# Performance work log

Hardware: AMD Instinct MI355X
Metric: run time of the kernel (lower is better)

## Reference

```python
import jax, jax.numpy as jnp
import numpy as np

QUALITY = 50.0
TEMP = 0.3  # soft-round temperature

_LUM = np.array([[16,11,10,16,24,40,51,61],[12,12,14,19,26,58,60,55],[14,13,16,24,40,57,69,56],[14,17,22,29,51,87,80,62],[18,22,37,56,68,109,103,77],[24,35,55,64,81,104,113,92],[49,64,78,87,103,121,120,101],[72,92,95,98,112,100,103,99]], dtype=np.float32)
_CHR = np.array([[17,18,24,47,99,99,99,99],[18,21,26,66,99,99,99,99],[24,26,56,99,99,99,99,99],[47,66,99,99,99,99,99,99],[99,99,99,99,99,99,99,99],[99,99,99,99,99,99,99,99],[99,99,99,99,99,99,99,99],[99,99,99,99,99,99,99,99]], dtype=np.float32)

def _scaled_qtable(base, qf):
    qf = max(1.0, min(100.0, qf))
    s = 5000.0 / qf if qf < 50 else 200.0 - 2.0 * qf
    return np.maximum(np.floor((base * s + 50.0) / 100.0), 1.0)

# Per-channel quantization tables: Y uses luminance, Cb/Cr use chrominance. (3,8,8)
QTAB = jnp.asarray(np.stack([_scaled_qtable(_LUM, QUALITY), _scaled_qtable(_CHR, QUALITY), _scaled_qtable(_CHR, QUALITY)]).astype(np.float32))

# The original 64x1x8x8 conv kernel factors as outer product D[u,x]*D[v,y].
_u = np.arange(8)[:, None]
_x = np.arange(8)[None, :]
_c = np.where(_u == 0, 1.0 / np.sqrt(2.0), 1.0)
DCT = jnp.asarray((0.5 * _c * np.cos((2 * _x + 1) * _u * np.pi / 16.0)).astype(np.float32))

M_FWD = jnp.array([[0.299, 0.587, 0.114], [-0.168736, -0.331264, 0.5], [0.5, -0.418688, -0.081312]], dtype=jnp.float32)
M_INV = jnp.array([[1.0, 0.0, 1.402], [1.0, -0.344136, -0.714136], [1.0, 1.772, 0.0]], dtype=jnp.float32)
OFF = jnp.array([0.0, 0.5, 0.5], dtype=jnp.float32)


def setup_inputs() -> dict:
    key = jax.random.key(0)
    x = jax.random.uniform(key, (32, 3, 512, 512), dtype=jnp.float32)
    return {"x": x}


def reference(x):
    B, C, H, W = x.shape  # H, W divisible by 8 (no pad branch)
    # RGB -> YCbCr, centered
    ycbcr = jnp.einsum('ij,bjhw->bihw', M_FWD, x) + OFF[None, :, None, None] - 0.5
    # split into 8x8 blocks: (B, 3, H/8, 8, W/8, 8)
    blocks = ycbcr.reshape(B, C, H // 8, 8, W // 8, 8)
    # block DCT: coef[u,v] = sum_{x,y} D[u,x] D[v,y] block[x,y]
    coef = jnp.einsum('ux,vy,bchxgy->bchugv', DCT, DCT, blocks)
    q = QTAB[None, :, None, :, None, :]  # broadcast per-channel table
    d = coef / q
    # smooth rounding: x + 0.5*tanh(50*T*(x - round(x)))
    sr = d + 0.5 * jnp.tanh(50.0 * TEMP * (d - jnp.round(d)))
    deq = sr * q
    # block IDCT (transpose of DCT): block[x,y] = sum_{u,v} D[u,x] D[v,y] coef[u,v]
    rec = jnp.einsum('ux,vy,bchugv->bchxgy', DCT, DCT, deq)
    ycbcr_rec = rec.reshape(B, C, H, W) + 0.5
    rgb = jnp.einsum('ij,bjhw->bihw', M_INV, ycbcr_rec - OFF[None, :, None, None])
    return jnp.clip(rgb, 0.0, 1.0)
```

## Files before the change

kernel.cpp:

```cpp
#include <hip/hip_runtime.h>
#include <math.h>

#define A0c 0.35355339059327373f
#define C1c 0.4903926402016152f
#define C2c 0.46193976625564337f
#define C3c 0.41573480615127262f
#define C5c 0.27778511650980114f
#define C6c 0.19134171618254492f
#define C7c 0.09754516100806417f

#define IMG_W 512
#define IMG_HW (512 * 512)

typedef float f8v __attribute__((ext_vector_type(8)));

__device__ const float QLUMT[64] = {
    16,12,14,14,18,24,49,72,
    11,12,13,17,22,35,64,92,
    10,14,16,22,37,55,78,95,
    16,19,24,29,56,64,87,98,
    24,26,40,51,68,81,103,112,
    40,58,57,87,109,104,121,100,
    51,60,69,80,103,113,120,103,
    61,55,56,62,77,92,101,99};
__device__ const float QCHRT[64] = {
    17,18,24,47,99,99,99,99,
    18,21,26,66,99,99,99,99,
    24,26,56,99,99,99,99,99,
    47,66,99,99,99,99,99,99,
    99,99,99,99,99,99,99,99,
    99,99,99,99,99,99,99,99,
    99,99,99,99,99,99,99,99,
    99,99,99,99,99,99,99,99};

__device__ __forceinline__ void fdct8(float v[8]) {
    float s0 = v[0] + v[7], s1 = v[1] + v[6], s2 = v[2] + v[5], s3 = v[3] + v[4];
    float d0 = v[0] - v[7], d1 = v[1] - v[6], d2 = v[2] - v[5], d3 = v[3] - v[4];
    float e0 = s0 + s3, e1 = s1 + s2, f0 = s0 - s3, f1 = s1 - s2;
    v[0] = A0c * (e0 + e1);
    v[4] = A0c * (e0 - e1);
    v[2] = C2c * f0 + C6c * f1;
    v[6] = C6c * f0 - C2c * f1;
    v[1] = C1c * d0 + C3c * d1 + C5c * d2 + C7c * d3;
    v[3] = C3c * d0 - C7c * d1 - C1c * d2 - C5c * d3;
    v[5] = C5c * d0 - C1c * d1 + C7c * d2 + C3c * d3;
    v[7] = C7c * d0 - C5c * d1 + C3c * d2 - C1c * d3;
}

__device__ __forceinline__ void idct8(float v[8]) {
    float g0 = v[0], g1 = v[1], g2 = v[2], g3 = v[3];
    float g4 = v[4], g5 = v[5], g6 = v[6], g7 = v[7];
    float ep = A0c * (g0 + g4), em = A0c * (g0 - g4);
    float t26a = C2c * g2 + C6c * g6;
    float t26b = C6c * g2 - C2c * g6;
    float e0 = ep + t26a, e1 = em + t26b, e2 = em - t26b, e3 = ep - t26a;
    float o0 = C1c * g1 + C3c * g3 + C5c * g5 + C7c * g7;
    float o1 = C3c * g1 - C7c * g3 - C1c * g5 - C5c * g7;
    float o2 = C5c * g1 - C1c * g3 + C7c * g5 + C3c * g7;
    float o3 = C7c * g1 - C5c * g3 + C3c * g5 - C1c * g7;
    v[0] = e0 + o0; v[7] = e0 - o0;
    v[1] = e1 + o1; v[6] = e1 - o1;
    v[2] = e2 + o2; v[5] = e2 - o2;
    v[3] = e3 + o3; v[4] = e3 - o3;
}

__device__ __forceinline__ float softq(float x, float q, float rq) {
    float d = x * rq;
    float rn = rintf(d);
    float t = d - rn;
    float e = __expf(-30.0f * fabsf(t));
    float th = (1.0f - e) * __builtin_amdgcn_rcpf(1.0f + e);
    th = copysignf(th, t);
    return (d + 0.5f * th) * q;
}

__device__ __forceinline__ void midchain(float w[8], const f8v q, const f8v rq) {
    fdct8(w);
#pragma unroll
    for (int u = 0; u < 8; ++u) w[u] = softq(w[u], q[u], rq[u]);
    idct8(w);
}

__device__ __forceinline__ void process_tile(const f8v Rv, const f8v Gv, const f8v Bv,
                                             float* xp0, float* xp1, float* xp2,
                                             int wi, int ri,
                                             const f8v qL, const f8v rqL,
                                             const f8v qC, const f8v rqC,
                                             float* obase) {
    float g0[8], g1[8], g2[8];
#pragma unroll
    for (int k = 0; k < 8; ++k) {
        float R = Rv[k], G = Gv[k], B = Bv[k];
        g0[k] = 0.299f * R + 0.587f * G + 0.114f * B - 0.5f;
        g1[k] = -0.168736f * R - 0.331264f * G + 0.5f * B;
        g2[k] = 0.5f * R - 0.418688f * G - 0.081312f * B;
    }
    fdct8(g0); fdct8(g1); fdct8(g2);

#pragma unroll
    for (int v = 0; v < 8; ++v) xp0[v * 72 + wi] = g0[v];
#pragma unroll
    for (int v = 0; v < 8; ++v) xp1[v * 72 + wi] = g1[v];
#pragma unroll
    for (int v = 0; v < 8; ++v) xp2[v * 72 + wi] = g2[v];

#pragma unroll
    for (int k = 0; k < 8; ++k) g0[k] = xp0[ri + k];
#pragma unroll
    for (int k = 0; k < 8; ++k) g1[k] = xp1[ri + k];
#pragma unroll
    for (int k = 0; k < 8; ++k) g2[k] = xp2[ri + k];

    midchain(g0, qL, rqL);
#pragma unroll
    for (int k = 0; k < 8; ++k) xp0[ri + k] = g0[k];
    midchain(g1, qC, rqC);
#pragma unroll
    for (int k = 0; k < 8; ++k) xp1[ri + k] = g1[k];
#pragma unroll
    for (int v = 0; v < 8; ++v) g0[v] = xp0[v * 72 + wi];
    midchain(g2, qC, rqC);
#pragma unroll
    for (int k = 0; k < 8; ++k) xp2[ri + k] = g2[k];
#pragma unroll
    for (int v = 0; v < 8; ++v) g1[v] = xp1[v * 72 + wi];
#pragma unroll
    for (int v = 0; v < 8; ++v) g2[v] = xp2[v * 72 + wi];

    idct8(g0); idct8(g1); idct8(g2);

    f8v Ro, Go, Bo;
#pragma unroll
    for (int k = 0; k < 8; ++k) {
        float Y  = g0[k] + 0.5f;
        float Cb = g1[k];
        float Cr = g2[k];
        float R = Y + 1.402f * Cr;
        float G = Y - 0.344136f * Cb - 0.714136f * Cr;
        float B = Y + 1.772f * Cb;
        Ro[k] = fminf(fmaxf(R, 0.0f), 1.0f);
        Go[k] = fminf(fmaxf(G, 0.0f), 1.0f);
        Bo[k] = fminf(fmaxf(B, 0.0f), 1.0f);
    }
    *(f8v*)(obase) = Ro;
    *(f8v*)(obase + IMG_HW) = Go;
    *(f8v*)(obase + 2 * IMG_HW) = Bo;
}

__global__ __launch_bounds__(256) void jpeg_kernel(const float* __restrict__ x,
                                                   float* __restrict__ out) {
    __shared__ float xpose[4][3][576];

    const int tid = threadIdx.x;
    const int wid = tid >> 6;
    const int lane = tid & 63;

    const int gw = blockIdx.x * 4 + wid;
    const int bimg = gw >> 9;
    const int rem = gw & 511;
    const int gh = rem >> 3;
    const int tx = rem & 7;

    const int blk = lane & 7;
    const int row = lane >> 3;

    const size_t off = (size_t)bimg * 3 * IMG_HW +
                       (size_t)(gh * 8 + row) * IMG_W + tx * 64 + blk * 8;
    const size_t toff = (size_t)16 * 3 * IMG_HW;

    const float* base0 = x + off;
    const float* base1 = base0 + toff;

    const f8v R0 = *(const f8v*)(base0);
    const f8v G0 = *(const f8v*)(base0 + IMG_HW);
    const f8v B0 = *(const f8v*)(base0 + 2 * IMG_HW);
    const f8v R1 = *(const f8v*)(base1);
    const f8v G1 = *(const f8v*)(base1 + IMG_HW);
    const f8v B1 = *(const f8v*)(base1 + 2 * IMG_HW);
    const f8v qL = *(const f8v*)&QLUMT[row * 8];
    const f8v qC = *(const f8v*)&QCHRT[row * 8];

    asm volatile("" ::: "memory");

    f8v rqL, rqC;
#pragma unroll
    for (int u = 0; u < 8; ++u) {
        rqL[u] = __builtin_amdgcn_rcpf(qL[u]);
        rqC[u] = __builtin_amdgcn_rcpf(qC[u]);
    }

    float* xp0 = xpose[wid][0];
    float* xp1 = xpose[wid][1];
    float* xp2 = xpose[wid][2];
    const int wi = blk * 9 + row;
    const int ri = row * 72 + blk * 9;

    process_tile(R0, G0, B0, xp0, xp1, xp2, wi, ri, qL, rqL, qC, rqC, out + off);
    process_tile(R1, G1, B1, xp0, xp1, xp2, wi, ri, qL, rqL, qC, rqC, out + off + toff);
}

extern "C" void kernel_launch(void* const* d_in, const int* in_sizes, int n_in,
                              void* d_out, int out_size, void* d_ws, size_t ws_size,
                              hipStream_t stream) {
    const float* x = (const float*)d_in[0];
    float* out = (float*)d_out;
    const int n_wg = 2048;
    hipLaunchKernelGGL(jpeg_kernel, dim3(n_wg), dim3(256), 0, stream, x, out);
}
```

Baseline: 39.89 us.

## Transpose 8x8 blocks in registers via DPP/swizzle instead of shared memory

Replaces the shared-memory transpose between row and column DCT passes with an in-register 8x8 transpose built from DPP row shuffles and ds_swizzle across the 8 lanes that hold a block. Lane mapping changes so each group of 8 consecutive lanes owns one block, and each thread now handles one tile instead of two, doubling the grid size. The soft-round tanh is also simplified to a single exp2-based expression without abs/copysign. The goal is to drop LDS traffic and its latency, at the cost of extra cross-lane moves and selects, and less per-thread load batching.

```diff
diff --git a/kernel.cpp b/kernel.cpp
--- a/kernel.cpp
+++ b/kernel.cpp
@@ -64,29 +64,74 @@
     v[3] = e3 + o3; v[4] = e3 - o3;
 }
 
+#define K_EXP2 43.2808512266689f
 __device__ __forceinline__ float softq(float x, float q, float rq) {
     float d = x * rq;
     float rn = rintf(d);
     float t = d - rn;
-    float e = __expf(-30.0f * fabsf(t));
-    float th = (1.0f - e) * __builtin_amdgcn_rcpf(1.0f + e);
-    th = copysignf(th, t);
+    float e2 = __builtin_amdgcn_exp2f(K_EXP2 * t);
+    float th = (e2 - 1.0f) * __builtin_amdgcn_rcpf(e2 + 1.0f);
     return (d + 0.5f * th) * q;
 }
 
-__device__ __forceinline__ void midchain(float w[8], const f8v q, const f8v rq) {
-    fdct8(w);
-#pragma unroll
-    for (int u = 0; u < 8; ++u) w[u] = softq(w[u], q[u], rq[u]);
-    idct8(w);
+template <int CTRL>
+__device__ __forceinline__ float fdpp(float x) {
+    return __int_as_float(__builtin_amdgcn_mov_dpp(__float_as_int(x), CTRL, 0xF, 0xF, false));
+}
+__device__ __forceinline__ float fswz4(float x) {
+    return __int_as_float(__builtin_amdgcn_ds_swizzle(__float_as_int(x), 0x101F));
 }
 
-__device__ __forceinline__ void process_tile(const f8v Rv, const f8v Gv, const f8v Bv,
-                                             float* xp0, float* xp1, float* xp2,
-                                             int wi, int ri,
-                                             const f8v qL, const f8v rqL,
-                                             const f8v qC, const f8v rqC,
-                                             float* obase) {
+__device__ __forceinline__ void xpose8(float v[8], bool rb0, bool rb1, bool rb2) {
+    float t[8];
+#pragma unroll
+    for (int i = 0; i < 8; ++i) t[i] = fdpp<0xB1>(v[i ^ 1]);
+#pragma unroll
+    for (int i = 0; i < 8; ++i) v[i] = (((i & 1) != 0) == rb0) ? v[i] : t[i];
+#pragma unroll
+    for (int i = 0; i < 8; ++i) t[i] = fdpp<0x4E>(v[i ^ 2]);
+#pragma unroll
+    for (int i = 0; i < 8; ++i) v[i] = (((i & 2) != 0) == rb1) ? v[i] : t[i];
+#pragma unroll
+    for (int i = 0; i < 8; ++i) t[i] = fswz4(v[i ^ 4]);
+#pragma unroll
+    for (int i = 0; i < 8; ++i) v[i] = (((i & 4) != 0) == rb2) ? v[i] : t[i];
+}
+
+__global__ __launch_bounds__(256) void jpeg_kernel(const float* __restrict__ x,
+                                                   float* __restrict__ out) {
+    const int tid = threadIdx.x;
+    const int wid = tid >> 6;
+    const int lane = tid & 63;
+
+    const int gw = blockIdx.x * 4 + wid;
+    const int bimg = gw >> 9;
+    const int rem = gw & 511;
+    const int gh = rem >> 3;
+    const int tx = rem & 7;
+
+    const int r = lane & 7;
+    const int blk = lane >> 3;
+
+    const bool rb0 = (r & 1) != 0, rb1 = (r & 2) != 0, rb2 = (r & 4) != 0;
+
+    const size_t off = (size_t)bimg * 3 * IMG_HW +
+                       (size_t)(gh * 8 + r) * IMG_W + tx * 64 + blk * 8;
+    const float* base = x + off;
+
+    const f8v Rv = *(const f8v*)(base);
+    const f8v Gv = *(const f8v*)(base + IMG_HW);
+    const f8v Bv = *(const f8v*)(base + 2 * IMG_HW);
+
+    const f8v qL = *(const f8v*)&QLUMT[r * 8];
+    const f8v qC = *(const f8v*)&QCHRT[r * 8];
+    f8v rqL, rqC;
+#pragma unroll
+    for (int u = 0; u < 8; ++u) {
+        rqL[u] = __builtin_amdgcn_rcpf(qL[u]);
+        rqC[u] = __builtin_amdgcn_rcpf(qC[u]);
+    }
+
     float g0[8], g1[8], g2[8];
 #pragma unroll
     for (int k = 0; k < 8; ++k) {
@@ -95,39 +140,33 @@
         g1[k] = -0.168736f * R - 0.331264f * G + 0.5f * B;
         g2[k] = 0.5f * R - 0.418688f * G - 0.081312f * B;
     }
-    fdct8(g0); fdct8(g1); fdct8(g2);
 
+    fdct8(g0);
+    xpose8(g0, rb0, rb1, rb2);
+    fdct8(g0);
 #pragma unroll
-    for (int v = 0; v < 8; ++v) xp0[v * 72 + wi] = g0[v];
+    for (int u = 0; u < 8; ++u) g0[u] = softq(g0[u], qL[u], rqL[u]);
+    idct8(g0);
+    xpose8(g0, rb0, rb1, rb2);
+    idct8(g0);
+
+    fdct8(g1);
+    xpose8(g1, rb0, rb1, rb2);
+    fdct8(g1);
 #pragma unroll
-    for (int v = 0; v < 8; ++v) xp1[v * 72 + wi] = g1[v];
+    for (int u = 0; u < 8; ++u) g1[u] = softq(g1[u], qC[u], rqC[u]);
+    idct8(g1);
+    xpose8(g1, rb0, rb1, rb2);
+    idct8(g1);
+
+    fdct8(g2);
+    xpose8(g2, rb0, rb1, rb2);
+    fdct8(g2);
 #pragma unroll
-    for (int v = 0; v < 8; ++v) xp2[v * 72 + wi] = g2[v];
-
-#pragma unroll
-    for (int k = 0; k < 8; ++k) g0[k] = xp0[ri + k];
-#pragma unroll
-    for (int k = 0; k < 8; ++k) g1[k] = xp1[ri + k];
-#pragma unroll
-    for (int k = 0; k < 8; ++k) g2[k] = xp2[ri + k];
-
-    midchain(g0, qL, rqL);
-#pragma unroll
-    for (int k = 0; k < 8; ++k) xp0[ri + k] = g0[k];
-    midchain(g1, qC, rqC);
-#pragma unroll
-    for (int k = 0; k < 8; ++k) xp1[ri + k] = g1[k];
-#pragma unroll
-    for (int v = 0; v < 8; ++v) g0[v] = xp0[v * 72 + wi];
-    midchain(g2, qC, rqC);
-#pragma unroll
-    for (int k = 0; k < 8; ++k) xp2[ri + k] = g2[k];
-#pragma unroll
-    for (int v = 0; v < 8; ++v) g1[v] = xp1[v * 72 + wi];
-#pragma unroll
-    for (int v = 0; v < 8; ++v) g2[v] = xp2[v * 72 + wi];
-
-    idct8(g0); idct8(g1); idct8(g2);
+    for (int u = 0; u < 8; ++u) g2[u] = softq(g2[u], qC[u], rqC[u]);
+    idct8(g2);
+    xpose8(g2, rb0, rb1, rb2);
+    idct8(g2);
 
     f8v Ro, Go, Bo;
 #pragma unroll
@@ -142,61 +181,10 @@
         Go[k] = fminf(fmaxf(G, 0.0f), 1.0f);
         Bo[k] = fminf(fmaxf(B, 0.0f), 1.0f);
     }
+    float* obase = out + off;
     *(f8v*)(obase) = Ro;
     *(f8v*)(obase + IMG_HW) = Go;
     *(f8v*)(obase + 2 * IMG_HW) = Bo;
-}
-
-__global__ __launch_bounds__(256) void jpeg_kernel(const float* __restrict__ x,
-                                                   float* __restrict__ out) {
-    __shared__ float xpose[4][3][576];
-
-    const int tid = threadIdx.x;
-    const int wid = tid >> 6;
-    const int lane = tid & 63;
-
-    const int gw = blockIdx.x * 4 + wid;
-    const int bimg = gw >> 9;
-    const int rem = gw & 511;
-    const int gh = rem >> 3;
-    const int tx = rem & 7;
-
-    const int blk = lane & 7;
-    const int row = lane >> 3;
-
-    const size_t off = (size_t)bimg * 3 * IMG_HW +
-                       (size_t)(gh * 8 + row) * IMG_W + tx * 64 + blk * 8;
-    const size_t toff = (size_t)16 * 3 * IMG_HW;
-
-    const float* base0 = x + off;
-    const float* base1 = base0 + toff;
-
-    const f8v R0 = *(const f8v*)(base0);
-    const f8v G0 = *(const f8v*)(base0 + IMG_HW);
-    const f8v B0 = *(const f8v*)(base0 + 2 * IMG_HW);
-    const f8v R1 = *(const f8v*)(base1);
-    const f8v G1 = *(const f8v*)(base1 + IMG_HW);
-    const f8v B1 = *(const f8v*)(base1 + 2 * IMG_HW);
-    const f8v qL = *(const f8v*)&QLUMT[row * 8];
-    const f8v qC = *(const f8v*)&QCHRT[row * 8];
-
-    asm volatile("" ::: "memory");
-
-    f8v rqL, rqC;
-#pragma unroll
-    for (int u = 0; u < 8; ++u) {
-        rqL[u] = __builtin_amdgcn_rcpf(qL[u]);
-        rqC[u] = __builtin_amdgcn_rcpf(qC[u]);
-    }
-
-    float* xp0 = xpose[wid][0];
-    float* xp1 = xpose[wid][1];
-    float* xp2 = xpose[wid][2];
-    const int wi = blk * 9 + row;
-    const int ri = row * 72 + blk * 9;
-
-    process_tile(R0, G0, B0, xp0, xp1, xp2, wi, ri, qL, rqL, qC, rqC, out + off);
-    process_tile(R1, G1, B1, xp0, xp1, xp2, wi, ri, qL, rqL, qC, rqC, out + off + toff);
 }
 
 extern "C" void kernel_launch(void* const* d_in, const int* in_sizes, int n_in,
@@ -204,6 +192,7 @@
                               hipStream_t stream) {
     const float* x = (const float*)d_in[0];
     float* out = (float*)d_out;
-    const int n_wg = 2048;
+    const int B = in_sizes[0] / (3 * IMG_HW);
+    const int n_wg = B * 128;
     hipLaunchKernelGGL(jpeg_kernel, dim3(n_wg), dim3(256), 0, stream, x, out);
 }
```

Result: slower. 46.35 us (+16.2%).
